# Performance work log

Hardware: AMD Instinct MI355X
Metric: run time of the kernel (lower is better)

Reference implementation:

```python
import jax, jax.numpy as jnp
import numpy as np

# Grid constants matching init_kwargs: spatial_shape=[32,128,128], Cin=16, Cout=32, k=3, stride=1, pad=1
D, H, W = 32, 128, 128
CIN, COUT = 16, 32
N_VOX = 200000


def _conv3d(x, w):
    # x: [B, D, H, W, C], w: [kd, kh, kw, Cin, Cout]
    return jax.lax.conv_general_dilated(
        x, w, window_strides=(1, 1, 1), padding='SAME',
        dimension_numbers=('NDHWC', 'DHWIO', 'NDHWC'))


def setup_inputs() -> dict:
    key = jax.random.key(0)
    k1, k2, k3, k4 = jax.random.split(key, 4)
    B = 4
    # unique active voxel coordinates (sparse tensors assume no duplicate coords)
    lin = jax.random.permutation(k1, B * D * H * W)[:N_VOX]
    b = lin // (D * H * W)
    r = lin % (D * H * W)
    z = r // (H * W)
    y = (r % (H * W)) // W
    x = r % W
    coors = jnp.stack([b, z, y, x], axis=1).astype(jnp.int32)  # [N, 4] (batch, z, y, x)
    features = jax.random.normal(k2, (N_VOX, CIN), jnp.float32)
    W1 = jax.random.normal(k3, (3, 3, 3, CIN, COUT), jnp.float32) * 0.05  # SparseConv3d weight
    W2 = jax.random.normal(k4, (3, 3, 3, COUT, CIN), jnp.float32) * 0.05  # SparseInverseConv3d weight
    return {'features': features, 'coors': coors, 'W1': W1, 'W2': W2, 'batch_size': 4}


def reference(features, coors, W1, W2, batch_size):
    b, z, y, x = coors[:, 0], coors[:, 1], coors[:, 2], coors[:, 3]
    # SparseConvTensor -> dense grid [B, D, H, W, Cin]
    dense = jnp.zeros((batch_size, D, H, W, CIN), features.dtype).at[b, z, y, x].add(features)
    # SparseConv3d (stride=1, pad=1): conv, active output set = kernel-dilation of input set
    h = _conv3d(dense, W1)  # [B, D, H, W, Cout]
    mask_in = jnp.zeros((batch_size, D, H, W, 1), features.dtype).at[b, z, y, x].set(1.0)
    mask_out = _conv3d(mask_in, jnp.ones((3, 3, 3, 1, 1), features.dtype)) > 0
    h = jnp.where(mask_out, h, 0.0)
    # SparseInverseConv3d with shared indice_key: transposed rulebook with flipped kernel
    # index; for stride=1/pad=1 this equals a same-padded conv restricted to original indices.
    out_dense = _conv3d(h, W2)  # [B, D, H, W, Cin]
    return out_dense[b, z, y, x]  # features of output SparseConvTensor at original coors
```

## Files before the change

kernel.cpp:

```cpp
#include <hip/hip_runtime.h>
#include <hip/hip_bf16.h>
#include <stdint.h>

#define D_ 32
#define H_ 128
#define W_ 128
#define NCIN 16
#define NCOUT 32
#define NVOX 200000
#define NB 4
#define PD (D_ + 4)
#define PH (H_ + 4)
#define PW (W_ + 4)

#define TZ 8
#define TY 16
#define TX 8
#define NTZ (D_ / TZ)
#define NTY (H_ / TY)
#define NTX (W_ / TX)
#define NTILES (NB * NTZ * NTY * NTX)
#define NKEY (NTILES * 27)

#define NCHUNK 64
#define MAXU 32768
#define MAIN_BLOCKS 1024
#define NWAVES (MAIN_BLOCKS * 4)

typedef __attribute__((ext_vector_type(8))) short bf16x8;
typedef __attribute__((ext_vector_type(4))) float f32x4;

__device__ __forceinline__ int vox_off(int b, int z, int y, int x) {
    return ((((b * PD + (z + 2)) * PH + (y + 2)) * PW + (x + 2))) * NCIN;
}
__device__ __forceinline__ int cls_of(int z, int y, int x) {
    int cz = (z == 0) ? 0 : ((z == D_ - 1) ? 2 : 1);
    int cy = (y == 0) ? 0 : ((y == H_ - 1) ? 2 : 1);
    int cx = (x == 0) ? 0 : ((x == W_ - 1) ? 2 : 1);
    return (cz * 3 + cy) * 3 + cx;
}
__device__ __forceinline__ int tile_of(int b, int z, int y, int x) {
    return ((b * NTZ + (z / TZ)) * NTY + (y / TY)) * NTX + (x / TX);
}

__global__ void wc_p_kernel(const float* __restrict__ W1, const float* __restrict__ W2,
                            float* __restrict__ P) {
    int k12 = blockIdx.x;
    int k1 = k12 / 27, k2 = k12 % 27;
    __shared__ float w1s[512], w2s[512];
    int t = threadIdx.x;
    w1s[t] = W1[k1 * 512 + t];       w1s[t + 256] = W1[k1 * 512 + 256 + t];
    w2s[t] = W2[k2 * 512 + t];       w2s[t + 256] = W2[k2 * 512 + 256 + t];
    __syncthreads();
    int ci = t >> 4, cf = t & 15;
    float acc = 0.f;
    #pragma unroll
    for (int cm = 0; cm < 32; ++cm)
        acc = fmaf(w1s[ci * 32 + cm], w2s[cm * 16 + cf], acc);
    P[k12 * 256 + t] = acc;
}

__global__ void wc_pack2_kernel(const float* __restrict__ P, __hip_bfloat16* __restrict__ WcB) {
    int blk = blockIdx.x;
    int cls = blk / NCHUNK, c = blk % NCHUNK;
    int t = threadIdx.x;
    int l = t >> 3, j = t & 7;
    int k = (l >> 4) * 8 + j;
    int ld = k >> 4, ci = k & 15, cf = l & 15;
    int delta = 2 * c + ld;
    float acc = 0.f;
    if (delta < 125) {
        int sz = delta / 25, sy = (delta / 5) % 5, sx = delta % 5;
        int cz = cls / 9, cy = (cls / 3) % 3, cx = cls % 3;
        for (int k1z = 0; k1z < 3; ++k1z) {
            int k2z = sz - k1z;
            if (k2z < 0 || k2z > 2) continue;
            if ((cz == 0 && k2z == 0) || (cz == 2 && k2z == 2)) continue;
            for (int k1y = 0; k1y < 3; ++k1y) {
                int k2y = sy - k1y;
                if (k2y < 0 || k2y > 2) continue;
                if ((cy == 0 && k2y == 0) || (cy == 2 && k2y == 2)) continue;
                for (int k1x = 0; k1x < 3; ++k1x) {
                    int k2x = sx - k1x;
                    if (k2x < 0 || k2x > 2) continue;
                    if ((cx == 0 && k2x == 0) || (cx == 2 && k2x == 2)) continue;
                    int k1 = (k1z * 3 + k1y) * 3 + k1x;
                    int k2 = (k2z * 3 + k2y) * 3 + k2x;
                    acc += P[(k1 * 27 + k2) * 256 + ci * 16 + cf];
                }
            }
        }
    }
    WcB[(size_t)blk * 512 + t] = __float2bfloat16(acc);
}

__global__ void scatter_count_kernel(const float* __restrict__ feats,
                                     const int* __restrict__ coors,
                                     __hip_bfloat16* __restrict__ dense,
                                     unsigned int* __restrict__ cnt) {
    int t = blockIdx.x * blockDim.x + threadIdx.x;
    if (t >= NVOX * NCIN) return;
    int v = t >> 4, c = t & 15;
    const int4* c4 = (const int4*)coors;
    int4 q = c4[v];
    dense[vox_off(q.x, q.y, q.z, q.w) + c] = __float2bfloat16(feats[t]);
    if (c == 0) {
        int key = tile_of(q.x, q.y, q.z, q.w) * 27 + cls_of(q.y, q.z, q.w);
        atomicAdd(&cnt[key], 1u);
    }
}

__global__ void tile_scan_kernel(const unsigned int* __restrict__ cnt,
                                 unsigned int* __restrict__ ucnt,
                                 unsigned int* __restrict__ vcnt) {
    int tile = blockIdx.x * blockDim.x + threadIdx.x;
    if (tile >= NTILES) return;
    unsigned uu = 0, vv = 0;
    for (int c = 0; c < 27; ++c) {
        unsigned cc = cnt[tile * 27 + c];
        uu += (cc + 63) >> 6;
        vv += cc;
    }
    ucnt[tile] = uu;
    vcnt[tile] = vv;
}

__global__ void scan2_kernel(const unsigned int* __restrict__ ucnt,
                             const unsigned int* __restrict__ vcnt,
                             unsigned int* __restrict__ ubase,
                             unsigned int* __restrict__ vbase,
                             unsigned int* __restrict__ ctrs) {
    __shared__ unsigned su[1024], sv[1024];
    int t = threadIdx.x;
    unsigned u0 = ucnt[2 * t], u1 = ucnt[2 * t + 1];
    unsigned v0 = vcnt[2 * t], v1 = vcnt[2 * t + 1];
    su[t] = u0 + u1; sv[t] = v0 + v1;
    __syncthreads();
    for (int o = 1; o < 1024; o <<= 1) {
        unsigned au = 0, av = 0;
        if (t >= o) { au = su[t - o]; av = sv[t - o]; }
        __syncthreads();
        su[t] += au; sv[t] += av;
        __syncthreads();
    }
    unsigned eu = su[t] - (u0 + u1);
    unsigned ev = sv[t] - (v0 + v1);
    ubase[2 * t] = eu; ubase[2 * t + 1] = eu + u0;
    vbase[2 * t] = ev; vbase[2 * t + 1] = ev + v0;
    if (t == 1023) { ctrs[2] = su[1023]; ctrs[0] = NWAVES; }
}

__global__ void emit_kernel(const unsigned int* __restrict__ cnt,
                            const unsigned int* __restrict__ ubase,
                            const unsigned int* __restrict__ vbase,
                            unsigned int* __restrict__ cur,
                            uint2* __restrict__ gdesc) {
    int tile = blockIdx.x * blockDim.x + threadIdx.x;
    if (tile >= NTILES) return;
    unsigned uo = ubase[tile], vo = vbase[tile];
    for (int c = 0; c < 27; ++c) {
        int key = tile * 27 + c;
        unsigned cc = cnt[key];
        cur[key] = vo;
        for (unsigned o = 0; o < cc; o += 64) {
            unsigned r = cc - o; if (r > 64) r = 64;
            if (uo < MAXU) gdesc[uo] = make_uint2(vo + o, (unsigned)c | (r << 16));
            ++uo;
        }
        vo += cc;
    }
}

__global__ void bucket_kernel(const int* __restrict__ coors,
                              unsigned int* __restrict__ cur,
                              unsigned int* __restrict__ list) {
    int v = blockIdx.x * blockDim.x + threadIdx.x;
    if (v >= NVOX) return;
    const int4* c4 = (const int4*)coors;
    int4 q = c4[v];
    int key = tile_of(q.x, q.y, q.z, q.w) * 27 + cls_of(q.y, q.z, q.w);
    unsigned pos = atomicAdd(&cur[key], 1u);
    list[pos] = (unsigned)v;
}

__global__ void __launch_bounds__(256, 4) main_kernel(
        const int* __restrict__ coors, const __hip_bfloat16* __restrict__ dense,
        const __hip_bfloat16* __restrict__ WcB, const uint2* __restrict__ gdesc,
        unsigned int* __restrict__ ctrs, const unsigned int* __restrict__ list,
        float* __restrict__ out) {
    __shared__ int lut[2 * NCHUNK];
    int t = threadIdx.x;
    if (t < 2 * NCHUNK) {
        int d = t, rel = 0;
        if (d < 125) {
            int dz = d / 25, dy = (d / 5) % 5, dx = d % 5;
            rel = (((dz - 2) * PH + (dy - 2)) * PW + (dx - 2)) * NCIN;
        }
        lut[t] = rel;
    }
    __syncthreads();
    unsigned nunits = ctrs[2];
    int w = t >> 6, lane = t & 63;
    int col = lane & 15, halfsel = (lane >> 4) & 1, dsel = lane >> 5;
    int bid = blockIdx.x;
    unsigned u = (unsigned)((bid & 7) * (NWAVES / 8) + (bid >> 3) * 4 + w);
    const int4* c4 = (const int4*)coors;

    while (u < nunits) {
        uint2 dsc = gdesc[u];
        unsigned off = dsc.x;
        int cls = (int)(dsc.y & 0xffffu);
        int cnt = (int)(dsc.y >> 16);

        int r0 = min(col, cnt - 1);
        int r1 = min(16 + col, cnt - 1);
        int r2 = min(32 + col, cnt - 1);
        int r3 = min(48 + col, cnt - 1);
        unsigned v0 = list[off + r0], v1 = list[off + r1];
        unsigned v2 = list[off + r2], v3 = list[off + r3];
        int4 q0 = c4[v0], q1 = c4[v1], q2 = c4[v2], q3 = c4[v3];
        int base0 = vox_off(q0.x, q0.y, q0.z, q0.w) + halfsel * 8;
        int base1 = vox_off(q1.x, q1.y, q1.z, q1.w) + halfsel * 8;
        int base2 = vox_off(q2.x, q2.y, q2.z, q2.w) + halfsel * 8;
        int base3 = vox_off(q3.x, q3.y, q3.z, q3.w) + halfsel * 8;
        const bf16x8* bq = (const bf16x8*)WcB + (size_t)cls * (NCHUNK * 64) + lane;

        f32x4 acc0 = {0.f, 0.f, 0.f, 0.f};
        f32x4 acc1 = {0.f, 0.f, 0.f, 0.f};
        f32x4 acc2 = {0.f, 0.f, 0.f, 0.f};
        f32x4 acc3 = {0.f, 0.f, 0.f, 0.f};
        bf16x8 bA, a0A, a1A, a2A, a3A, bB, a0B, a1B, a2B, a3B;

#define LOADS(c_, BV, A0, A1, A2, A3) { \
        int cc_ = (c_) & (NCHUNK - 1); \
        int rel_ = lut[2 * cc_ + dsel]; \
        A0 = *(const bf16x8*)(dense + (base0 + rel_)); \
        A1 = *(const bf16x8*)(dense + (base1 + rel_)); \
        A2 = *(const bf16x8*)(dense + (base2 + rel_)); \
        A3 = *(const bf16x8*)(dense + (base3 + rel_)); \
        BV = bq[cc_ * 64]; }

        LOADS(0, bA, a0A, a1A, a2A, a3A)
        LOADS(1, bB, a0B, a1B, a2B, a3B)
        for (int c = 0; c < NCHUNK; c += 2) {
            acc0 = __builtin_amdgcn_mfma_f32_16x16x32_bf16(a0A, bA, acc0, 0, 0, 0);
            acc1 = __builtin_amdgcn_mfma_f32_16x16x32_bf16(a1A, bA, acc1, 0, 0, 0);
            acc2 = __builtin_amdgcn_mfma_f32_16x16x32_bf16(a2A, bA, acc2, 0, 0, 0);
            acc3 = __builtin_amdgcn_mfma_f32_16x16x32_bf16(a3A, bA, acc3, 0, 0, 0);
            LOADS(c + 2, bA, a0A, a1A, a2A, a3A)
            acc0 = __builtin_amdgcn_mfma_f32_16x16x32_bf16(a0B, bB, acc0, 0, 0, 0);
            acc1 = __builtin_amdgcn_mfma_f32_16x16x32_bf16(a1B, bB, acc1, 0, 0, 0);
            acc2 = __builtin_amdgcn_mfma_f32_16x16x32_bf16(a2B, bB, acc2, 0, 0, 0);
            acc3 = __builtin_amdgcn_mfma_f32_16x16x32_bf16(a3B, bB, acc3, 0, 0, 0);
            LOADS(c + 3, bB, a0B, a1B, a2B, a3B)
        }
#undef LOADS

        int rowq = (lane >> 4) * 4;
#define WRITEJ(j_, ACC) { \
        int orow_ = 16 * (j_) + rowq; \
        _Pragma("unroll") \
        for (int reg = 0; reg < 4; ++reg) { \
            int rr_ = orow_ + reg; \
            if (rr_ < cnt) { \
                unsigned vo_ = list[off + rr_]; \
                out[(size_t)vo_ * 16 + col] = ACC[reg]; \
            } } }
        WRITEJ(0, acc0)
        WRITEJ(1, acc1)
        WRITEJ(2, acc2)
        WRITEJ(3, acc3)
#undef WRITEJ

        unsigned nu = 0;
        if (lane == 0) nu = atomicAdd(&ctrs[0], 1u);
        u = (unsigned)__shfl((int)nu, 0);
    }
}

extern "C" void kernel_launch(void* const* d_in, const int* in_sizes, int n_in,
                              void* d_out, int out_size, void* d_ws, size_t ws_size,
                              hipStream_t stream) {
    const float* features = (const float*)d_in[0];
    const int*   coors    = (const int*)d_in[1];
    const float* W1       = (const float*)d_in[2];
    const float* W2       = (const float*)d_in[3];
    float* out = (float*)d_out;

    const size_t dense_elems = (size_t)NB * PD * PH * PW * NCIN;
    const size_t dense_bytes = dense_elems * sizeof(__hip_bfloat16);
    char* p = (char*)d_ws;
    __hip_bfloat16* dense = (__hip_bfloat16*)p;
    p += ((dense_bytes + 255) / 256) * 256;
    __hip_bfloat16* WcB = (__hip_bfloat16*)p;
    p += (((size_t)27 * NCHUNK * 512 * 2 + 255) / 256) * 256;
    unsigned int* cnt = (unsigned int*)p;
    p += (((size_t)NKEY * 4 + 255) / 256) * 256;
    unsigned int* cur = (unsigned int*)p;
    p += (((size_t)NKEY * 4 + 255) / 256) * 256;
    unsigned int* ucnt = (unsigned int*)p;  p += 8192;
    unsigned int* vcnt = (unsigned int*)p;  p += 8192;
    unsigned int* ubase = (unsigned int*)p; p += 8192;
    unsigned int* vbase = (unsigned int*)p; p += 8192;
    unsigned int* ctrs = (unsigned int*)p;  p += 256;
    unsigned int* list = (unsigned int*)p;
    float* P = (float*)list;
    p += (((size_t)NVOX * 4 + 255) / 256) * 256;
    uint2* gdesc = (uint2*)p;

    hipMemsetAsync(dense, 0, dense_bytes, stream);
    hipMemsetAsync(cnt, 0, (size_t)NKEY * 4, stream);

    wc_p_kernel<<<729, 256, 0, stream>>>(W1, W2, P);
    wc_pack2_kernel<<<27 * NCHUNK, 512, 0, stream>>>(P, WcB);
    scatter_count_kernel<<<(NVOX * NCIN + 255) / 256, 256, 0, stream>>>(features, coors, dense, cnt);
    tile_scan_kernel<<<NTILES / 256, 256, 0, stream>>>(cnt, ucnt, vcnt);
    scan2_kernel<<<1, 1024, 0, stream>>>(ucnt, vcnt, ubase, vbase, ctrs);
    emit_kernel<<<NTILES / 256, 256, 0, stream>>>(cnt, ubase, vbase, cur, gdesc);
    bucket_kernel<<<(NVOX + 255) / 256, 256, 0, stream>>>(coors, cur, list);
    main_kernel<<<MAIN_BLOCKS, 256, 0, stream>>>(coors, dense, WcB, gdesc, ctrs, list, out);
}
```

Baseline: 276.6 us.

## Stage per-tile halo in LDS and process 16-voxel groups per tile block

Replaces the persistent work-queue main kernel, which gathers A operands straight from global memory, with one block per 8x8x8 tile. Each block first copies a 12x12x12 bf16 halo into shared memory with global_load_lds, then runs 16-row MFMA groups that read their A fragments from LDS using a 5x5x3 chunk layout. The three-kernel scan/emit chain becomes a single prep kernel with fixed per-tile descriptor capacity. The intent is to replace scattered global gathers with reuse from LDS. In exchange it uses 16-row groups, a padded fifth dx column (75 chunks instead of 63), lower occupancy and fixed per-tile capacity limits.

```diff
diff --git a/kernel.cpp b/kernel.cpp
--- a/kernel.cpp
+++ b/kernel.cpp
@@ -13,19 +13,14 @@
 #define PH (H_ + 4)
 #define PW (W_ + 4)
 
-#define TZ 8
-#define TY 16
-#define TX 8
-#define NTZ (D_ / TZ)
-#define NTY (H_ / TY)
-#define NTX (W_ / TX)
+#define NTZ 4
+#define NTY 16
+#define NTX 16
 #define NTILES (NB * NTZ * NTY * NTX)
 #define NKEY (NTILES * 27)
-
-#define NCHUNK 64
-#define MAXU 32768
-#define MAIN_BLOCKS 1024
-#define NWAVES (MAIN_BLOCKS * 4)
+#define GCAP 64
+#define HALO_BYTES 55296
+#define NCHUNK 75
 
 typedef __attribute__((ext_vector_type(8))) short bf16x8;
 typedef __attribute__((ext_vector_type(4))) float f32x4;
@@ -40,7 +35,7 @@
     return (cz * 3 + cy) * 3 + cx;
 }
 __device__ __forceinline__ int tile_of(int b, int z, int y, int x) {
-    return ((b * NTZ + (z / TZ)) * NTY + (y / TY)) * NTX + (x / TX);
+    return ((b * NTZ + (z >> 3)) * NTY + (y >> 3)) * NTX + (x >> 3);
 }
 
 __global__ void wc_p_kernel(const float* __restrict__ W1, const float* __restrict__ W2,
@@ -62,15 +57,17 @@
 
 __global__ void wc_pack2_kernel(const float* __restrict__ P, __hip_bfloat16* __restrict__ WcB) {
     int blk = blockIdx.x;
-    int cls = blk / NCHUNK, c = blk % NCHUNK;
-    int t = threadIdx.x;
-    int l = t >> 3, j = t & 7;
-    int k = (l >> 4) * 8 + j;
+    int cls = blk / NCHUNK, rj = blk % NCHUNK;
+    int r = rj / 3, j = rj % 3;
+    int dz = r / 5, dy = r % 5;
+    int t = threadIdx.x;
+    int l = t >> 3, jj = t & 7;
+    int k = (l >> 4) * 8 + jj;
     int ld = k >> 4, ci = k & 15, cf = l & 15;
-    int delta = 2 * c + ld;
+    int dx = 2 * j + ld;
     float acc = 0.f;
-    if (delta < 125) {
-        int sz = delta / 25, sy = (delta / 5) % 5, sx = delta % 5;
+    if (dx < 5) {
+        int sz = dz, sy = dy, sx = dx;
         int cz = cls / 9, cy = (cls / 3) % 3, cx = cls % 3;
         for (int k1z = 0; k1z < 3; ++k1z) {
             int k2z = sz - k1z;
@@ -110,64 +107,41 @@
     }
 }
 
-__global__ void tile_scan_kernel(const unsigned int* __restrict__ cnt,
-                                 unsigned int* __restrict__ ucnt,
-                                 unsigned int* __restrict__ vcnt) {
-    int tile = blockIdx.x * blockDim.x + threadIdx.x;
-    if (tile >= NTILES) return;
-    unsigned uu = 0, vv = 0;
-    for (int c = 0; c < 27; ++c) {
-        unsigned cc = cnt[tile * 27 + c];
-        uu += (cc + 63) >> 6;
-        vv += cc;
-    }
-    ucnt[tile] = uu;
-    vcnt[tile] = vv;
-}
-
-__global__ void scan2_kernel(const unsigned int* __restrict__ ucnt,
-                             const unsigned int* __restrict__ vcnt,
-                             unsigned int* __restrict__ ubase,
-                             unsigned int* __restrict__ vbase,
-                             unsigned int* __restrict__ ctrs) {
-    __shared__ unsigned su[1024], sv[1024];
-    int t = threadIdx.x;
-    unsigned u0 = ucnt[2 * t], u1 = ucnt[2 * t + 1];
-    unsigned v0 = vcnt[2 * t], v1 = vcnt[2 * t + 1];
-    su[t] = u0 + u1; sv[t] = v0 + v1;
+__global__ void prep_kernel(const unsigned int* __restrict__ cnt,
+                            unsigned int* __restrict__ cur,
+                            uint2* __restrict__ gdesc,
+                            unsigned int* __restrict__ ngroups) {
+    __shared__ unsigned sv[1024];
+    int t = threadIdx.x;
+    unsigned tot = 0;
+    for (int i = 0; i < 4; ++i) {
+        int tile = t * 4 + i;
+        for (int c = 0; c < 27; ++c) tot += cnt[tile * 27 + c];
+    }
+    sv[t] = tot;
     __syncthreads();
     for (int o = 1; o < 1024; o <<= 1) {
-        unsigned au = 0, av = 0;
-        if (t >= o) { au = su[t - o]; av = sv[t - o]; }
+        unsigned a = (t >= o) ? sv[t - o] : 0u;
         __syncthreads();
-        su[t] += au; sv[t] += av;
+        sv[t] += a;
         __syncthreads();
     }
-    unsigned eu = su[t] - (u0 + u1);
-    unsigned ev = sv[t] - (v0 + v1);
-    ubase[2 * t] = eu; ubase[2 * t + 1] = eu + u0;
-    vbase[2 * t] = ev; vbase[2 * t + 1] = ev + v0;
-    if (t == 1023) { ctrs[2] = su[1023]; ctrs[0] = NWAVES; }
-}
-
-__global__ void emit_kernel(const unsigned int* __restrict__ cnt,
-                            const unsigned int* __restrict__ ubase,
-                            const unsigned int* __restrict__ vbase,
-                            unsigned int* __restrict__ cur,
-                            uint2* __restrict__ gdesc) {
-    int tile = blockIdx.x * blockDim.x + threadIdx.x;
-    if (tile >= NTILES) return;
-    unsigned uo = ubase[tile], vo = vbase[tile];
-    for (int c = 0; c < 27; ++c) {
-        int key = tile * 27 + c;
-        unsigned cc = cnt[key];
-        cur[key] = vo;
-        for (unsigned o = 0; o < cc; o += 64) {
-            unsigned r = cc - o; if (r > 64) r = 64;
-            if (uo < MAXU) gdesc[uo] = make_uint2(vo + o, (unsigned)c | (r << 16));
-            ++uo;
-        }
-        vo += cc;
+    unsigned vo = sv[t] - tot;
+    for (int i = 0; i < 4; ++i) {
+        int tile = t * 4 + i;
+        unsigned g = 0;
+        for (int c = 0; c < 27; ++c) {
+            int key = tile * 27 + c;
+            unsigned cc = cnt[key];
+            cur[key] = vo;
+            for (unsigned o2 = 0; o2 < cc; o2 += 16) {
+                unsigned r = cc - o2; if (r > 16) r = 16;
+                gdesc[tile * GCAP + g] = make_uint2(vo + o2, (unsigned)c | (r << 16));
+                ++g;
+            }
+            vo += cc;
+        }
+        ngroups[tile] = g;
     }
 }
 
@@ -183,98 +157,83 @@
     list[pos] = (unsigned)v;
 }
 
-__global__ void __launch_bounds__(256, 4) main_kernel(
+__global__ void __launch_bounds__(256, 2) main_kernel(
         const int* __restrict__ coors, const __hip_bfloat16* __restrict__ dense,
         const __hip_bfloat16* __restrict__ WcB, const uint2* __restrict__ gdesc,
-        unsigned int* __restrict__ ctrs, const unsigned int* __restrict__ list,
+        const unsigned int* __restrict__ ngroups, const unsigned int* __restrict__ list,
         float* __restrict__ out) {
-    __shared__ int lut[2 * NCHUNK];
-    int t = threadIdx.x;
-    if (t < 2 * NCHUNK) {
-        int d = t, rel = 0;
-        if (d < 125) {
-            int dz = d / 25, dy = (d / 5) % 5, dx = d % 5;
-            rel = (((dz - 2) * PH + (dy - 2)) * PW + (dx - 2)) * NCIN;
-        }
-        lut[t] = rel;
-    }
-    __syncthreads();
-    unsigned nunits = ctrs[2];
+    __shared__ uint4 halo4[(HALO_BYTES + 64) / 16];
+    unsigned char* halo = (unsigned char*)halo4;
+    int t = threadIdx.x;
     int w = t >> 6, lane = t & 63;
     int col = lane & 15, halfsel = (lane >> 4) & 1, dsel = lane >> 5;
+
     int bid = blockIdx.x;
-    unsigned u = (unsigned)((bid & 7) * (NWAVES / 8) + (bid >> 3) * 4 + w);
+    int tid = (bid & 7) * (NTILES / 8) + (bid >> 3);
+    int ng = (int)ngroups[tid];
+    if (ng == 0) return;
+    int tx = tid & 15, r1 = tid >> 4;
+    int ty = r1 & 15, r2 = r1 >> 4;
+    int tz = r2 & 3, b = r2 >> 2;
+    int pz = tz * 8, py = ty * 8, px = tx * 8;
+
+    for (int i = 0; i < 27; ++i) {
+        int hw = i * 4 + w;
+        int hc = hw * 64 + lane;
+        int cell = hc >> 1, half = hc & 1;
+        int cz = cell / 144;
+        int rc = cell - cz * 144;
+        int cy = rc / 12;
+        int cx = rc - cy * 12;
+        const __hip_bfloat16* gp = dense +
+            (((b * PD + pz + cz) * PH + (py + cy)) * PW + (px + cx)) * NCIN + half * 8;
+        __builtin_amdgcn_global_load_lds(
+            (const __attribute__((address_space(1))) void*)gp,
+            (__attribute__((address_space(3))) void*)(halo + hw * 1024), 16, 0, 0);
+    }
+    if (t < 4) halo4[3456 + t] = make_uint4(0u, 0u, 0u, 0u);
+    __syncthreads();
+
     const int4* c4 = (const int4*)coors;
-
-    while (u < nunits) {
-        uint2 dsc = gdesc[u];
+    for (int g = w; g < ng; g += 4) {
+        uint2 dsc = gdesc[tid * GCAP + g];
         unsigned off = dsc.x;
         int cls = (int)(dsc.y & 0xffffu);
         int cnt = (int)(dsc.y >> 16);
-
-        int r0 = min(col, cnt - 1);
-        int r1 = min(16 + col, cnt - 1);
-        int r2 = min(32 + col, cnt - 1);
-        int r3 = min(48 + col, cnt - 1);
-        unsigned v0 = list[off + r0], v1 = list[off + r1];
-        unsigned v2 = list[off + r2], v3 = list[off + r3];
-        int4 q0 = c4[v0], q1 = c4[v1], q2 = c4[v2], q3 = c4[v3];
-        int base0 = vox_off(q0.x, q0.y, q0.z, q0.w) + halfsel * 8;
-        int base1 = vox_off(q1.x, q1.y, q1.z, q1.w) + halfsel * 8;
-        int base2 = vox_off(q2.x, q2.y, q2.z, q2.w) + halfsel * 8;
-        int base3 = vox_off(q3.x, q3.y, q3.z, q3.w) + halfsel * 8;
+        int rr = min(col, cnt - 1);
+        unsigned v = list[off + rr];
+        int4 q = c4[v];
+        int vz = q.y - pz, vy = q.z - py, vx = q.w - px;
+        int abase = ((vz * 12 + vy) * 12 + vx) * 32 + dsel * 32 + halfsel * 16;
         const bf16x8* bq = (const bf16x8*)WcB + (size_t)cls * (NCHUNK * 64) + lane;
 
-        f32x4 acc0 = {0.f, 0.f, 0.f, 0.f};
-        f32x4 acc1 = {0.f, 0.f, 0.f, 0.f};
-        f32x4 acc2 = {0.f, 0.f, 0.f, 0.f};
-        f32x4 acc3 = {0.f, 0.f, 0.f, 0.f};
-        bf16x8 bA, a0A, a1A, a2A, a3A, bB, a0B, a1B, a2B, a3B;
-
-#define LOADS(c_, BV, A0, A1, A2, A3) { \
-        int cc_ = (c_) & (NCHUNK - 1); \
-        int rel_ = lut[2 * cc_ + dsel]; \
-        A0 = *(const bf16x8*)(dense + (base0 + rel_)); \
-        A1 = *(const bf16x8*)(dense + (base1 + rel_)); \
-        A2 = *(const bf16x8*)(dense + (base2 + rel_)); \
-        A3 = *(const bf16x8*)(dense + (base3 + rel_)); \
-        BV = bq[cc_ * 64]; }
-
-        LOADS(0, bA, a0A, a1A, a2A, a3A)
-        LOADS(1, bB, a0B, a1B, a2B, a3B)
-        for (int c = 0; c < NCHUNK; c += 2) {
-            acc0 = __builtin_amdgcn_mfma_f32_16x16x32_bf16(a0A, bA, acc0, 0, 0, 0);
-            acc1 = __builtin_amdgcn_mfma_f32_16x16x32_bf16(a1A, bA, acc1, 0, 0, 0);
-            acc2 = __builtin_amdgcn_mfma_f32_16x16x32_bf16(a2A, bA, acc2, 0, 0, 0);
-            acc3 = __builtin_amdgcn_mfma_f32_16x16x32_bf16(a3A, bA, acc3, 0, 0, 0);
-            LOADS(c + 2, bA, a0A, a1A, a2A, a3A)
-            acc0 = __builtin_amdgcn_mfma_f32_16x16x32_bf16(a0B, bB, acc0, 0, 0, 0);
-            acc1 = __builtin_amdgcn_mfma_f32_16x16x32_bf16(a1B, bB, acc1, 0, 0, 0);
-            acc2 = __builtin_amdgcn_mfma_f32_16x16x32_bf16(a2B, bB, acc2, 0, 0, 0);
-            acc3 = __builtin_amdgcn_mfma_f32_16x16x32_bf16(a3B, bB, acc3, 0, 0, 0);
-            LOADS(c + 3, bB, a0B, a1B, a2B, a3B)
-        }
-#undef LOADS
-
+        f32x4 acc = {0.f, 0.f, 0.f, 0.f};
+        #pragma unroll 1
+        for (int dz = 0; dz < 5; ++dz) {
+            #pragma unroll
+            for (int dy = 0; dy < 5; ++dy) {
+                int ab = abase + (dz * 144 + dy * 12) * 32;
+                bf16x8 a0 = *(const bf16x8*)(halo + ab);
+                bf16x8 a1 = *(const bf16x8*)(halo + ab + 64);
+                bf16x8 a2 = *(const bf16x8*)(halo + ab + 128);
+                int ci0 = (dz * 5 + dy) * 3;
+                bf16x8 b0 = bq[ci0 * 64];
+                bf16x8 b1 = bq[ci0 * 64 + 64];
+                bf16x8 b2 = bq[ci0 * 64 + 128];
+                acc = __builtin_amdgcn_mfma_f32_16x16x32_bf16(a0, b0, acc, 0, 0, 0);
+                acc = __builtin_amdgcn_mfma_f32_16x16x32_bf16(a1, b1, acc, 0, 0, 0);
+                acc = __builtin_amdgcn_mfma_f32_16x16x32_bf16(a2, b2, acc, 0, 0, 0);
+            }
+        }
         int rowq = (lane >> 4) * 4;
-#define WRITEJ(j_, ACC) { \
-        int orow_ = 16 * (j_) + rowq; \
-        _Pragma("unroll") \
-        for (int reg = 0; reg < 4; ++reg) { \
-            int rr_ = orow_ + reg; \
-            if (rr_ < cnt) { \
-                unsigned vo_ = list[off + rr_]; \
-                out[(size_t)vo_ * 16 + col] = ACC[reg]; \
-            } } }
-        WRITEJ(0, acc0)
-        WRITEJ(1, acc1)
-        WRITEJ(2, acc2)
-        WRITEJ(3, acc3)
-#undef WRITEJ
-
-        unsigned nu = 0;
-        if (lane == 0) nu = atomicAdd(&ctrs[0], 1u);
-        u = (unsigned)__shfl((int)nu, 0);
+        #pragma unroll
+        for (int reg = 0; reg < 4; ++reg) {
+            int orow = rowq + reg;
+            if (orow < cnt) {
+                unsigned vo = list[off + orow];
+                out[(size_t)vo * 16 + col] = acc[reg];
+            }
+        }
     }
 }
 
@@ -298,15 +257,11 @@
     p += (((size_t)NKEY * 4 + 255) / 256) * 256;
     unsigned int* cur = (unsigned int*)p;
     p += (((size_t)NKEY * 4 + 255) / 256) * 256;
-    unsigned int* ucnt = (unsigned int*)p;  p += 8192;
-    unsigned int* vcnt = (unsigned int*)p;  p += 8192;
-    unsigned int* ubase = (unsigned int*)p; p += 8192;
-    unsigned int* vbase = (unsigned int*)p; p += 8192;
-    unsigned int* ctrs = (unsigned int*)p;  p += 256;
+    unsigned int* ngroups = (unsigned int*)p; p += NTILES * 4;
+    uint2* gdesc = (uint2*)p;
+    p += (size_t)NTILES * GCAP * 8;
     unsigned int* list = (unsigned int*)p;
     float* P = (float*)list;
-    p += (((size_t)NVOX * 4 + 255) / 256) * 256;
-    uint2* gdesc = (uint2*)p;
 
     hipMemsetAsync(dense, 0, dense_bytes, stream);
     hipMemsetAsync(cnt, 0, (size_t)NKEY * 4, stream);
@@ -314,9 +269,7 @@
     wc_p_kernel<<<729, 256, 0, stream>>>(W1, W2, P);
     wc_pack2_kernel<<<27 * NCHUNK, 512, 0, stream>>>(P, WcB);
     scatter_count_kernel<<<(NVOX * NCIN + 255) / 256, 256, 0, stream>>>(features, coors, dense, cnt);
-    tile_scan_kernel<<<NTILES / 256, 256, 0, stream>>>(cnt, ucnt, vcnt);
-    scan2_kernel<<<1, 1024, 0, stream>>>(ucnt, vcnt, ubase, vbase, ctrs);
-    emit_kernel<<<NTILES / 256, 256, 0, stream>>>(cnt, ubase, vbase, cur, gdesc);
+    prep_kernel<<<1, 1024, 0, stream>>>(cnt, cur, gdesc, ngroups);
     bucket_kernel<<<(NVOX + 255) / 256, 256, 0, stream>>>(coors, cur, list);
-    main_kernel<<<MAIN_BLOCKS, 256, 0, stream>>>(coors, dense, WcB, gdesc, ctrs, list, out);
-}
+    main_kernel<<<NTILES, 256, 0, stream>>>(coors, dense, WcB, gdesc, ngroups, list, out);
+}
```

New measurement: 382.8 us. 1.38x slower.
